# Kernel optimization log

Measured on AMD Instinct MI355X. Metric: run time of the kernel, lower is better.

## Reference

```python
import jax, jax.numpy as jnp
import numpy as np

N_HEADS = 16

def _rope_tables(L, head_dim, dtype):
    inv_freq = 1.0 / (10000.0 ** (jnp.arange(0, head_dim, 2, dtype=jnp.float32) / head_dim))
    t = jnp.arange(L, dtype=jnp.float32)
    freqs = jnp.outer(t, inv_freq)            # [L, head_dim/2]
    emb = jnp.concatenate([freqs, freqs], -1)  # [L, head_dim]
    return jnp.cos(emb).astype(dtype), jnp.sin(emb).astype(dtype)

def _apply_rope(x, cos, sin):
    # x: [B, L, H, hd]; cos/sin: [1, L, 1, hd]
    half = x.shape[-1] // 2
    x1, x2 = x[..., :half], x[..., half:]
    x_rot = jnp.concatenate([-x2, x1], -1)
    return x * cos + x_rot * sin

def setup_inputs() -> dict:
    key = jax.random.key(0)
    ks = jax.random.split(key, 5)
    D = 1024
    s = 0.02
    return {
        "x": jax.random.normal(ks[0], (4, 2048, D), jnp.float32),
        "w_qkv": jax.random.normal(ks[1], (3 * D, D), jnp.float32) * s,
        "b_qkv": jax.random.normal(ks[2], (3 * D,), jnp.float32) * s,
        "w_out": jax.random.normal(ks[3], (D, D), jnp.float32) * s,
        "b_out": jax.random.normal(ks[4], (D,), jnp.float32) * s,
    }

def reference(x, w_qkv, b_qkv, w_out, b_out):
    B, L, D = x.shape
    H = N_HEADS
    hd = D // H
    scale = hd ** -0.5
    qkv = (x @ w_qkv.T + b_qkv).reshape(B, L, 3, H, hd)
    q, k, v = qkv[:, :, 0], qkv[:, :, 1], qkv[:, :, 2]  # [B,L,H,hd]
    cos, sin = _rope_tables(L, hd, x.dtype)
    cos = cos[None, :, None, :]
    sin = sin[None, :, None, :]
    q = _apply_rope(q, cos, sin)
    k = _apply_rope(k, cos, sin)
    # [B,H,L,L] scores, non-causal softmax
    attn = jnp.einsum('blhd,bmhd->bhlm', q, k) * scale
    attn = jax.nn.softmax(attn, axis=-1)
    out = jnp.einsum('bhlm,bmhd->blhd', attn, v).reshape(B, L, D)
    return out @ w_out.T + b_out
```

## Files before the change

kernel.cpp:

```cpp
#include <hip/hip_runtime.h>
#include <stdint.h>

typedef __attribute__((ext_vector_type(4))) float f32x4;
typedef __attribute__((ext_vector_type(8))) short bf16x8;
typedef __attribute__((ext_vector_type(4))) short s16x4;
typedef __attribute__((ext_vector_type(4))) float fp32x4;

#define QSCALE 0.18033688f

__device__ __forceinline__ short f2bf(float f) {
    union { float f; unsigned u; } v; v.f = f;
    unsigned u = v.u;
    unsigned r = u + 0x7fffu + ((u >> 16) & 1u);
    return (short)(r >> 16);
}
__device__ __forceinline__ unsigned cvtpk(float a, float b) {
    unsigned r;
    asm("v_cvt_pk_bf16_f32 %0, %1, %2" : "=v"(r) : "v"(a), "v"(b));
    return r;
}

__device__ __forceinline__ void gld_lds16(const void* g, void* l) {
    __builtin_amdgcn_global_load_lds(
        (const __attribute__((address_space(1))) unsigned int*)(uintptr_t)g,
        (__attribute__((address_space(3))) unsigned int*)(uintptr_t)l,
        16, 0, 0);
}

__global__ __launch_bounds__(256) void prep_kernel(const float* __restrict__ x,
                                                   const float* __restrict__ wq,
                                                   const float* __restrict__ wo,
                                                   short* __restrict__ xb,
                                                   short* __restrict__ wqb,
                                                   short* __restrict__ wob,
                                                   float* __restrict__ tab) {
    int bid = blockIdx.x, tid = threadIdx.x;
    if (bid < 6144) {
        const float* in; short* out; int base;
        if (bid < 4096)      { in = x;  out = xb;  base = bid; }
        else if (bid < 5632) { in = wq; out = wqb; base = bid - 4096; }
        else                 { in = wo; out = wob; base = bid - 5632; }
        int idx = (base * 256 + tid) * 8;
        fp32x4 a = *(const fp32x4*)&in[idx];
        fp32x4 b = *(const fp32x4*)&in[idx + 4];
        union { unsigned w[4]; bf16x8 v; } u;
        u.w[0] = cvtpk(a[0], a[1]); u.w[1] = cvtpk(a[2], a[3]);
        u.w[2] = cvtpk(b[0], b[1]); u.w[3] = cvtpk(b[2], b[3]);
        *(bf16x8*)&out[idx] = u.v;
    } else {
        int idx = (bid - 6144) * 256 + tid;
        int l = idx >> 5, d = idx & 31;
        float inv = expf(-(float)d / 32.f * logf(10000.f));
        float ang = (float)l * inv;
        tab[idx * 2 + 0] = cosf(ang);
        tab[idx * 2 + 1] = sinf(ang);
    }
}

template<int MODE>
__global__ __launch_bounds__(512, 2)
void gemm_bt(const short* __restrict__ A,
             const short* __restrict__ B,
             const float* __restrict__ bias,
             void* __restrict__ Cout,
             short* __restrict__ VTout,
             const float* __restrict__ tab,
             int M, int N, int K) {
    __shared__ short lds[3 * 24576];
    const int tid = threadIdx.x;
    const int lane = tid & 63, wave = tid >> 6;
    const int i15 = lane & 15, g = lane >> 4;
    const int wr = wave >> 1, wc = wave & 1;

    const int nbx = gridDim.x;
    const int nwg = nbx * gridDim.y;
    int bid = blockIdx.y * nbx + blockIdx.x;
    int sw = (bid & 7) * (nwg >> 3) + (bid >> 3);
    const int m0 = (sw / nbx) * 256;
    const int n0 = (sw % nbx) * 128;

    const int xr3 = i15 & 3, xb2 = (i15 >> 2) & 1;
    const int cLo = g ^ xr3;
    const int aoff0 = (wr * 64 + i15) * 64 + (xb2 * 4 + cLo) * 8;
    const int aoff1 = (wr * 64 + i15) * 64 + ((1 ^ xb2) * 4 + cLo) * 8;
    const int boff0 = (wc * 64 + i15) * 64 + (xb2 * 4 + cLo) * 8;
    const int boff1 = (wc * 64 + i15) * 64 + ((1 ^ xb2) * 4 + cLo) * 8;

    const int srow = tid >> 3;
    const int ss = (tid & 7) ^ (srow & 7);
    const short* a0 = A + (size_t)(m0 + srow) * K + ss * 8;
    const short* a1 = a0 + (size_t)64 * K;
    const short* a2 = a0 + (size_t)128 * K;
    const short* a3 = a0 + (size_t)192 * K;
    const short* b0 = B + (size_t)(n0 + srow) * K + ss * 8;
    const short* b1 = b0 + (size_t)64 * K;

#define ST_A(slot, r, p) do { gld_lds16(p, lds + (slot) * 24576 + ((r) * 512 + wave * 64) * 8); p += 64; } while (0)
#define ST_B(slot, r, p) do { gld_lds16(p, lds + (slot) * 24576 + 16384 + ((r) * 512 + wave * 64) * 8); p += 64; } while (0)

    ST_A(0, 0, a0); ST_A(0, 1, a1); ST_B(0, 0, b0);
    ST_A(0, 2, a2); ST_A(0, 3, a3); ST_B(0, 1, b1);
    ST_A(1, 0, a0); ST_A(1, 1, a1); ST_B(1, 0, b0);
    ST_A(1, 2, a2); ST_A(1, 3, a3); ST_B(1, 1, b1);

    f32x4 acc[4][4] = {};
    const int NT = K >> 6;
    int slc = 0;

    for (int T = 0; T < NT; ++T) {
        int stslot = slc + 2; if (stslot >= 3) stslot -= 3;
        if (T == NT - 1) asm volatile("s_waitcnt vmcnt(0)" ::: "memory");
        else             asm volatile("s_waitcnt vmcnt(6)" ::: "memory");
        __builtin_amdgcn_s_barrier();
        __builtin_amdgcn_sched_barrier(0);

        if (T + 2 < NT) {
            ST_A(stslot, 0, a0); ST_A(stslot, 1, a1);
            ST_A(stslot, 2, a2); ST_A(stslot, 3, a3);
            ST_B(stslot, 0, b0); ST_B(stslot, 1, b1);
        }

        const short* As_ = lds + slc * 24576;
        const short* Bs_ = As_ + 16384;
        bf16x8 af[4][2], bfr[4][2];
#pragma unroll
        for (int m = 0; m < 4; ++m) {
            af[m][0] = *(const bf16x8*)&As_[aoff0 + m * 1024];
            af[m][1] = *(const bf16x8*)&As_[aoff1 + m * 1024];
        }
#pragma unroll
        for (int n = 0; n < 4; ++n) {
            bfr[n][0] = *(const bf16x8*)&Bs_[boff0 + n * 1024];
            bfr[n][1] = *(const bf16x8*)&Bs_[boff1 + n * 1024];
        }
        __builtin_amdgcn_s_setprio(1);
#pragma unroll
        for (int m = 0; m < 4; ++m)
#pragma unroll
            for (int n = 0; n < 4; ++n)
#pragma unroll
                for (int ks = 0; ks < 2; ++ks)
                    acc[m][n] = __builtin_amdgcn_mfma_f32_16x16x32_bf16(af[m][ks], bfr[n][ks], acc[m][n], 0, 0, 0);
        __builtin_amdgcn_s_setprio(0);

        slc = (slc == 2) ? 0 : slc + 1;
    }
#undef ST_A
#undef ST_B

    if (MODE == 0) {
#pragma unroll
        for (int m = 0; m < 4; ++m)
#pragma unroll
            for (int n = 0; n < 4; ++n) {
                int col = n0 + wc * 64 + n * 16 + i15;
                float bcol = bias[col];
#pragma unroll
                for (int j = 0; j < 4; ++j) {
                    int row = m0 + wr * 64 + m * 16 + g * 4 + j;
                    ((float*)Cout)[(size_t)row * N + col] = acc[m][n][j] + bcol;
                }
            }
    } else {
        const int sec = n0 >> 10;
        if (sec < 2) {
            const float qs = (sec == 0) ? QSCALE : 1.0f;
            short* out = (short*)Cout;
#pragma unroll
            for (int m = 0; m < 4; ++m) {
#pragma unroll
                for (int pp = 0; pp < 2; ++pp) {
                    int d = pp * 16 + i15;
                    int collo = n0 + wc * 64 + pp * 16 + i15;
                    float blo = bias[collo], bhi = bias[collo + 32];
#pragma unroll
                    for (int j = 0; j < 4; ++j) {
                        int row = m0 + wr * 64 + m * 16 + g * 4 + j;
                        int l = row & 2047;
                        float2 cs = *(const float2*)&tab[(l * 32 + d) * 2];
                        float x1 = acc[m][pp][j] + blo;
                        float x2 = acc[m][pp + 2][j] + bhi;
                        out[(size_t)row * 3072 + collo]      = f2bf((x1 * cs.x - x2 * cs.y) * qs);
                        out[(size_t)row * 3072 + collo + 32] = f2bf((x2 * cs.x + x1 * cs.y) * qs);
                    }
                }
            }
        } else {
#pragma unroll
            for (int m = 0; m < 4; ++m) {
                int rbase = m0 + wr * 64 + m * 16 + g * 4;
                int lbase = rbase & 2047, bidx = rbase >> 11;
#pragma unroll
                for (int n = 0; n < 4; ++n) {
                    int vcol = (n0 - 2048) + wc * 64 + n * 16 + i15;
                    int h = vcol >> 6, d = vcol & 63;
                    float bb = bias[n0 + wc * 64 + n * 16 + i15];
                    union { unsigned w[2]; s16x4 v; } u;
                    u.w[0] = cvtpk(acc[m][n][0] + bb, acc[m][n][1] + bb);
                    u.w[1] = cvtpk(acc[m][n][2] + bb, acc[m][n][3] + bb);
                    *(s16x4*)&VTout[((size_t)(bidx * 16 + h) * 64 + d) * 2048 + lbase] = u.v;
                }
            }
        }
    }
}

__global__ __launch_bounds__(512, 8) void attn_kernel(const short* __restrict__ qkv,
                                                      const short* __restrict__ VT,
                                                      short* __restrict__ O) {
    __shared__ short Ks[2][64 * 64];
    __shared__ short Vs[2][64 * 64];
    int orig = blockIdx.x;
    int xcd = orig & 7, idx = orig >> 3;
    int bh = xcd * 8 + (idx >> 4), qt = idx & 15;
    int b = bh >> 4, h = bh & 15;
    int tid = threadIdx.x, lane = tid & 63, wave = tid >> 6;
    int i15 = lane & 15, g = lane >> 4;
    int q0 = qt * 128;

    size_t qrow = (size_t)(b * 2048 + q0 + wave * 16 + i15);
    bf16x8 qf[2];
    qf[0] = *(const bf16x8*)&qkv[qrow * 3072 + h * 64 + 0  + g * 8];
    qf[1] = *(const bf16x8*)&qkv[qrow * 3072 + h * 64 + 32 + g * 8];

    bf16x8 onesf;
#pragma unroll
    for (int e = 0; e < 8; ++e) onesf[e] = (short)0x3F80;

    const int srow = tid >> 3, ss8 = (tid & 7) ^ (srow & 7);
    const int sprow = (srow & 0x23) | ((srow & 0x10) >> 2) | ((srow & 0x0C) << 1);
    const short* kp = qkv + (size_t)(b * 2048) * 3072 + 1024 + h * 64
                      + (size_t)sprow * 3072 + ss8 * 8;
    const short* vp = VT + (size_t)bh * 64 * 2048 + (size_t)srow * 2048 + ss8 * 8;

    const int xr3 = i15 & 3, xb2 = (i15 >> 2) & 1;
    const int cLo = g ^ xr3;
    const int o0 = i15 * 64 + (xb2 * 4 + cLo) * 8;
    const int o1 = i15 * 64 + ((1 ^ xb2) * 4 + cLo) * 8;

    f32x4 acc_o[4] = {};
    f32x4 acc_l = {0.f, 0.f, 0.f, 0.f};

#define STAGE(bk, bv)                                        \
    do {                                                     \
        gld_lds16(kp, (bk) + wave * 512);                    \
        gld_lds16(vp, (bv) + wave * 512);                    \
        kp += 64 * 3072;                                     \
        vp += 64;                                            \
    } while (0)

    STAGE(Ks[0], Vs[0]);

    for (int t = 0; t < 32; ++t) {
        const int cur = t & 1;
        if (t > 0) {
            __builtin_amdgcn_s_barrier();
            __builtin_amdgcn_sched_barrier(0);
        }
        if (t + 1 < 32) {
            STAGE(Ks[cur ^ 1], Vs[cur ^ 1]);
            asm volatile("s_waitcnt vmcnt(2)" ::: "memory");
        } else {
            asm volatile("s_waitcnt vmcnt(0)" ::: "memory");
        }
        __builtin_amdgcn_s_barrier();
        __builtin_amdgcn_sched_barrier(0);

        const short* ks = Ks[cur];
        const short* vs = Vs[cur];

        f32x4 sa[4] = {};
        __builtin_amdgcn_s_setprio(1);
#pragma unroll
        for (int kb = 0; kb < 2; ++kb) {
            const int ko = kb ? o1 : o0;
#pragma unroll
            for (int jb = 0; jb < 4; ++jb) {
                bf16x8 kf = *(const bf16x8*)&ks[ko + jb * 1024];
                sa[jb] = __builtin_amdgcn_mfma_f32_16x16x32_bf16(kf, qf[kb], sa[jb], 0, 0, 0);
            }
        }
        __builtin_amdgcn_s_setprio(0);

        float p[4][4];
#pragma unroll
        for (int jb = 0; jb < 4; ++jb)
#pragma unroll
            for (int r = 0; r < 4; ++r)
                p[jb][r] = __builtin_amdgcn_exp2f(sa[jb][r]);

        bf16x8 pf[2];
#pragma unroll
        for (int kb = 0; kb < 2; ++kb) {
            union { unsigned w[4]; bf16x8 v; } u;
            u.w[0] = cvtpk(p[2 * kb][0],     p[2 * kb][1]);
            u.w[1] = cvtpk(p[2 * kb][2],     p[2 * kb][3]);
            u.w[2] = cvtpk(p[2 * kb + 1][0], p[2 * kb + 1][1]);
            u.w[3] = cvtpk(p[2 * kb + 1][2], p[2 * kb + 1][3]);
            pf[kb] = u.v;
        }

        __builtin_amdgcn_s_setprio(1);
#pragma unroll
        for (int db = 0; db < 4; ++db) {
#pragma unroll
            for (int kb = 0; kb < 2; ++kb) {
                bf16x8 vf = *(const bf16x8*)&vs[(kb ? o1 : o0) + db * 1024];
                acc_o[db] = __builtin_amdgcn_mfma_f32_16x16x32_bf16(pf[kb], vf, acc_o[db], 0, 0, 0);
            }
        }
        acc_l = __builtin_amdgcn_mfma_f32_16x16x32_bf16(pf[0], onesf, acc_l, 0, 0, 0);
        acc_l = __builtin_amdgcn_mfma_f32_16x16x32_bf16(pf[1], onesf, acc_l, 0, 0, 0);
        __builtin_amdgcn_s_setprio(0);
    }
#undef STAGE

    float linv4[4];
#pragma unroll
    for (int r = 0; r < 4; ++r) linv4[r] = 1.f / acc_l[r];
#pragma unroll
    for (int db = 0; db < 4; ++db) {
        int ocol = h * 64 + db * 16 + i15;
#pragma unroll
        for (int r = 0; r < 4; ++r) {
            int orow = b * 2048 + q0 + wave * 16 + g * 4 + r;
            O[(size_t)orow * 1024 + ocol] = f2bf(acc_o[db][r] * linv4[r]);
        }
    }
}

extern "C" void kernel_launch(void* const* d_in, const int* in_sizes, int n_in,
                              void* d_out, int out_size, void* d_ws, size_t ws_size,
                              hipStream_t stream) {
    const float* x     = (const float*)d_in[0];
    const float* w_qkv = (const float*)d_in[1];
    const float* b_qkv = (const float*)d_in[2];
    const float* w_out = (const float*)d_in[3];
    const float* b_out = (const float*)d_in[4];

    char* ws = (char*)d_ws;
    short* qkvb = (short*)(ws);
    short* xb   = (short*)(ws + 50331648);
    short* wqb  = (short*)(ws + 67108864);
    short* wob  = (short*)(ws + 73400320);
    short* VT   = (short*)(ws + 75497472);
    float* rt   = (float*)(ws + 92274688);
    short* Ob   = xb;

    prep_kernel<<<6400, 256, 0, stream>>>(x, w_qkv, w_out, xb, wqb, wob, rt);

    gemm_bt<1><<<dim3(24, 32), 512, 0, stream>>>(xb, wqb, b_qkv, qkvb, VT, rt, 8192, 3072, 1024);
    attn_kernel<<<1024, 512, 0, stream>>>(qkvb, VT, Ob);
    gemm_bt<0><<<dim3(8, 32), 512, 0, stream>>>(Ob, wob, b_out, d_out, nullptr, nullptr, 8192, 1024, 1024);
}
```

Baseline: 171.1 us.

## Shrink GEMM tiles to 128x128 with 4 waves and give attention waves 32 query rows

The GEMM moves from 512-thread 256x128 tiles with a 3-slot LDS ring to 256-thread 128x128 tiles with double buffering, and the grid doubles in M. The attention kernel now runs 4 waves per block, each handling two 16-row query groups, so every K/V fragment read from LDS is reused twice. Each thread stages twice as many K/V rows per tile. The aim is better reuse and a better occupancy/latency balance, at the cost of more registers per wave and shallower prefetch in the GEMM.

```diff
diff --git a/kernel.cpp b/kernel.cpp
--- a/kernel.cpp
+++ b/kernel.cpp
@@ -58,7 +58,7 @@
 }
 
 template<int MODE>
-__global__ __launch_bounds__(512, 2)
+__global__ __launch_bounds__(256, 2)
 void gemm_bt(const short* __restrict__ A,
              const short* __restrict__ B,
              const float* __restrict__ bias,
@@ -66,7 +66,7 @@
              short* __restrict__ VTout,
              const float* __restrict__ tab,
              int M, int N, int K) {
-    __shared__ short lds[3 * 24576];
+    __shared__ short lds[2 * 16384];
     const int tid = threadIdx.x;
     const int lane = tid & 63, wave = tid >> 6;
     const int i15 = lane & 15, g = lane >> 4;
@@ -76,7 +76,7 @@
     const int nwg = nbx * gridDim.y;
     int bid = blockIdx.y * nbx + blockIdx.x;
     int sw = (bid & 7) * (nwg >> 3) + (bid >> 3);
-    const int m0 = (sw / nbx) * 256;
+    const int m0 = (sw / nbx) * 128;
     const int n0 = (sw % nbx) * 128;
 
     const int xr3 = i15 & 3, xb2 = (i15 >> 2) & 1;
@@ -89,39 +89,50 @@
     const int srow = tid >> 3;
     const int ss = (tid & 7) ^ (srow & 7);
     const short* a0 = A + (size_t)(m0 + srow) * K + ss * 8;
-    const short* a1 = a0 + (size_t)64 * K;
-    const short* a2 = a0 + (size_t)128 * K;
-    const short* a3 = a0 + (size_t)192 * K;
+    const short* a1 = a0 + (size_t)32 * K;
+    const short* a2 = a0 + (size_t)64 * K;
+    const short* a3 = a0 + (size_t)96 * K;
     const short* b0 = B + (size_t)(n0 + srow) * K + ss * 8;
-    const short* b1 = b0 + (size_t)64 * K;
-
-#define ST_A(slot, r, p) do { gld_lds16(p, lds + (slot) * 24576 + ((r) * 512 + wave * 64) * 8); p += 64; } while (0)
-#define ST_B(slot, r, p) do { gld_lds16(p, lds + (slot) * 24576 + 16384 + ((r) * 512 + wave * 64) * 8); p += 64; } while (0)
-
-    ST_A(0, 0, a0); ST_A(0, 1, a1); ST_B(0, 0, b0);
-    ST_A(0, 2, a2); ST_A(0, 3, a3); ST_B(0, 1, b1);
-    ST_A(1, 0, a0); ST_A(1, 1, a1); ST_B(1, 0, b0);
-    ST_A(1, 2, a2); ST_A(1, 3, a3); ST_B(1, 1, b1);
+    const short* b1 = b0 + (size_t)32 * K;
+    const short* b2 = b0 + (size_t)64 * K;
+    const short* b3 = b0 + (size_t)96 * K;
+
+#define STAGE(slot)                                                       \
+    do {                                                                  \
+        gld_lds16(a0, lds + (slot) * 16384 + 0 * 2048 + wave * 512);      \
+        gld_lds16(a1, lds + (slot) * 16384 + 1 * 2048 + wave * 512);      \
+        gld_lds16(a2, lds + (slot) * 16384 + 2 * 2048 + wave * 512);      \
+        gld_lds16(a3, lds + (slot) * 16384 + 3 * 2048 + wave * 512);      \
+        gld_lds16(b0, lds + (slot) * 16384 + 8192 + 0 * 2048 + wave * 512); \
+        gld_lds16(b1, lds + (slot) * 16384 + 8192 + 1 * 2048 + wave * 512); \
+        gld_lds16(b2, lds + (slot) * 16384 + 8192 + 2 * 2048 + wave * 512); \
+        gld_lds16(b3, lds + (slot) * 16384 + 8192 + 3 * 2048 + wave * 512); \
+        a0 += 64; a1 += 64; a2 += 64; a3 += 64;                           \
+        b0 += 64; b1 += 64; b2 += 64; b3 += 64;                           \
+    } while (0)
+
+    STAGE(0);
 
     f32x4 acc[4][4] = {};
     const int NT = K >> 6;
-    int slc = 0;
 
     for (int T = 0; T < NT; ++T) {
-        int stslot = slc + 2; if (stslot >= 3) stslot -= 3;
-        if (T == NT - 1) asm volatile("s_waitcnt vmcnt(0)" ::: "memory");
-        else             asm volatile("s_waitcnt vmcnt(6)" ::: "memory");
+        const int cur = T & 1;
+        if (T > 0) {
+            __builtin_amdgcn_s_barrier();
+            __builtin_amdgcn_sched_barrier(0);
+        }
+        if (T + 1 < NT) {
+            STAGE(cur ^ 1);
+            asm volatile("s_waitcnt vmcnt(8)" ::: "memory");
+        } else {
+            asm volatile("s_waitcnt vmcnt(0)" ::: "memory");
+        }
         __builtin_amdgcn_s_barrier();
         __builtin_amdgcn_sched_barrier(0);
 
-        if (T + 2 < NT) {
-            ST_A(stslot, 0, a0); ST_A(stslot, 1, a1);
-            ST_A(stslot, 2, a2); ST_A(stslot, 3, a3);
-            ST_B(stslot, 0, b0); ST_B(stslot, 1, b1);
-        }
-
-        const short* As_ = lds + slc * 24576;
-        const short* Bs_ = As_ + 16384;
+        const short* As_ = lds + cur * 16384;
+        const short* Bs_ = As_ + 8192;
         bf16x8 af[4][2], bfr[4][2];
 #pragma unroll
         for (int m = 0; m < 4; ++m) {
@@ -142,11 +153,8 @@
                 for (int ks = 0; ks < 2; ++ks)
                     acc[m][n] = __builtin_amdgcn_mfma_f32_16x16x32_bf16(af[m][ks], bfr[n][ks], acc[m][n], 0, 0, 0);
         __builtin_amdgcn_s_setprio(0);
-
-        slc = (slc == 2) ? 0 : slc + 1;
-    }
-#undef ST_A
-#undef ST_B
+    }
+#undef STAGE
 
     if (MODE == 0) {
 #pragma unroll
@@ -205,7 +213,7 @@
     }
 }
 
-__global__ __launch_bounds__(512, 8) void attn_kernel(const short* __restrict__ qkv,
+__global__ __launch_bounds__(256, 4) void attn_kernel(const short* __restrict__ qkv,
                                                       const short* __restrict__ VT,
                                                       short* __restrict__ O) {
     __shared__ short Ks[2][64 * 64];
@@ -218,35 +226,46 @@
     int i15 = lane & 15, g = lane >> 4;
     int q0 = qt * 128;
 
-    size_t qrow = (size_t)(b * 2048 + q0 + wave * 16 + i15);
-    bf16x8 qf[2];
-    qf[0] = *(const bf16x8*)&qkv[qrow * 3072 + h * 64 + 0  + g * 8];
-    qf[1] = *(const bf16x8*)&qkv[qrow * 3072 + h * 64 + 32 + g * 8];
+    size_t qbase = (size_t)(b * 2048 + q0 + wave * 32);
+    bf16x8 qf[2][2];
+#pragma unroll
+    for (int qg = 0; qg < 2; ++qg) {
+        qf[qg][0] = *(const bf16x8*)&qkv[(qbase + qg * 16 + i15) * 3072 + h * 64 + 0  + g * 8];
+        qf[qg][1] = *(const bf16x8*)&qkv[(qbase + qg * 16 + i15) * 3072 + h * 64 + 32 + g * 8];
+    }
 
     bf16x8 onesf;
 #pragma unroll
     for (int e = 0; e < 8; ++e) onesf[e] = (short)0x3F80;
 
-    const int srow = tid >> 3, ss8 = (tid & 7) ^ (srow & 7);
-    const int sprow = (srow & 0x23) | ((srow & 0x10) >> 2) | ((srow & 0x0C) << 1);
-    const short* kp = qkv + (size_t)(b * 2048) * 3072 + 1024 + h * 64
-                      + (size_t)sprow * 3072 + ss8 * 8;
-    const short* vp = VT + (size_t)bh * 64 * 2048 + (size_t)srow * 2048 + ss8 * 8;
+    const int srow = tid >> 3;
+    const int ss8 = (tid & 7) ^ (srow & 7);
+    const int pr0 = (srow & 0x23) | ((srow & 0x10) >> 2) | ((srow & 0x0C) << 1);
+    const int sr1 = srow + 32;
+    const int pr1 = (sr1 & 0x23) | ((sr1 & 0x10) >> 2) | ((sr1 & 0x0C) << 1);
+    const short* kb_ = qkv + (size_t)(b * 2048) * 3072 + 1024 + h * 64 + ss8 * 8;
+    const short* kp0 = kb_ + (size_t)pr0 * 3072;
+    const short* kp1 = kb_ + (size_t)pr1 * 3072;
+    const short* vb_ = VT + (size_t)bh * 64 * 2048 + ss8 * 8;
+    const short* vp0 = vb_ + (size_t)srow * 2048;
+    const short* vp1 = vb_ + (size_t)sr1 * 2048;
 
     const int xr3 = i15 & 3, xb2 = (i15 >> 2) & 1;
     const int cLo = g ^ xr3;
     const int o0 = i15 * 64 + (xb2 * 4 + cLo) * 8;
     const int o1 = i15 * 64 + ((1 ^ xb2) * 4 + cLo) * 8;
 
-    f32x4 acc_o[4] = {};
-    f32x4 acc_l = {0.f, 0.f, 0.f, 0.f};
+    f32x4 acc_o[2][4] = {};
+    f32x4 acc_l[2] = {};
 
 #define STAGE(bk, bv)                                        \
     do {                                                     \
-        gld_lds16(kp, (bk) + wave * 512);                    \
-        gld_lds16(vp, (bv) + wave * 512);                    \
-        kp += 64 * 3072;                                     \
-        vp += 64;                                            \
+        gld_lds16(kp0, (bk) + wave * 512);                   \
+        gld_lds16(kp1, (bk) + 2048 + wave * 512);            \
+        gld_lds16(vp0, (bv) + wave * 512);                   \
+        gld_lds16(vp1, (bv) + 2048 + wave * 512);            \
+        kp0 += (size_t)64 * 3072; kp1 += (size_t)64 * 3072;  \
+        vp0 += 64; vp1 += 64;                                \
     } while (0)
 
     STAGE(Ks[0], Vs[0]);
@@ -259,7 +278,7 @@
         }
         if (t + 1 < 32) {
             STAGE(Ks[cur ^ 1], Vs[cur ^ 1]);
-            asm volatile("s_waitcnt vmcnt(2)" ::: "memory");
+            asm volatile("s_waitcnt vmcnt(4)" ::: "memory");
         } else {
             asm volatile("s_waitcnt vmcnt(0)" ::: "memory");
         }
@@ -269,35 +288,40 @@
         const short* ks = Ks[cur];
         const short* vs = Vs[cur];
 
-        f32x4 sa[4] = {};
+        f32x4 sa[2][4] = {};
         __builtin_amdgcn_s_setprio(1);
 #pragma unroll
         for (int kb = 0; kb < 2; ++kb) {
             const int ko = kb ? o1 : o0;
-#pragma unroll
-            for (int jb = 0; jb < 4; ++jb) {
-                bf16x8 kf = *(const bf16x8*)&ks[ko + jb * 1024];
-                sa[jb] = __builtin_amdgcn_mfma_f32_16x16x32_bf16(kf, qf[kb], sa[jb], 0, 0, 0);
-            }
+            bf16x8 kf[4];
+#pragma unroll
+            for (int jb = 0; jb < 4; ++jb) kf[jb] = *(const bf16x8*)&ks[ko + jb * 1024];
+#pragma unroll
+            for (int qg = 0; qg < 2; ++qg)
+#pragma unroll
+                for (int jb = 0; jb < 4; ++jb)
+                    sa[qg][jb] = __builtin_amdgcn_mfma_f32_16x16x32_bf16(kf[jb], qf[qg][kb], sa[qg][jb], 0, 0, 0);
         }
         __builtin_amdgcn_s_setprio(0);
 
-        float p[4][4];
-#pragma unroll
-        for (int jb = 0; jb < 4; ++jb)
-#pragma unroll
-            for (int r = 0; r < 4; ++r)
-                p[jb][r] = __builtin_amdgcn_exp2f(sa[jb][r]);
-
-        bf16x8 pf[2];
-#pragma unroll
-        for (int kb = 0; kb < 2; ++kb) {
-            union { unsigned w[4]; bf16x8 v; } u;
-            u.w[0] = cvtpk(p[2 * kb][0],     p[2 * kb][1]);
-            u.w[1] = cvtpk(p[2 * kb][2],     p[2 * kb][3]);
-            u.w[2] = cvtpk(p[2 * kb + 1][0], p[2 * kb + 1][1]);
-            u.w[3] = cvtpk(p[2 * kb + 1][2], p[2 * kb + 1][3]);
-            pf[kb] = u.v;
+        bf16x8 pf[2][2];
+#pragma unroll
+        for (int qg = 0; qg < 2; ++qg) {
+            float p[4][4];
+#pragma unroll
+            for (int jb = 0; jb < 4; ++jb)
+#pragma unroll
+                for (int r = 0; r < 4; ++r)
+                    p[jb][r] = __builtin_amdgcn_exp2f(sa[qg][jb][r]);
+#pragma unroll
+            for (int kb = 0; kb < 2; ++kb) {
+                union { unsigned w[4]; bf16x8 v; } u;
+                u.w[0] = cvtpk(p[2 * kb][0],     p[2 * kb][1]);
+                u.w[1] = cvtpk(p[2 * kb][2],     p[2 * kb][3]);
+                u.w[2] = cvtpk(p[2 * kb + 1][0], p[2 * kb + 1][1]);
+                u.w[3] = cvtpk(p[2 * kb + 1][2], p[2 * kb + 1][3]);
+                pf[qg][kb] = u.v;
+            }
         }
 
         __builtin_amdgcn_s_setprio(1);
@@ -306,25 +330,33 @@
 #pragma unroll
             for (int kb = 0; kb < 2; ++kb) {
                 bf16x8 vf = *(const bf16x8*)&vs[(kb ? o1 : o0) + db * 1024];
-                acc_o[db] = __builtin_amdgcn_mfma_f32_16x16x32_bf16(pf[kb], vf, acc_o[db], 0, 0, 0);
-            }
-        }
-        acc_l = __builtin_amdgcn_mfma_f32_16x16x32_bf16(pf[0], onesf, acc_l, 0, 0, 0);
-        acc_l = __builtin_amdgcn_mfma_f32_16x16x32_bf16(pf[1], onesf, acc_l, 0, 0, 0);
+#pragma unroll
+                for (int qg = 0; qg < 2; ++qg)
+                    acc_o[qg][db] = __builtin_amdgcn_mfma_f32_16x16x32_bf16(pf[qg][kb], vf, acc_o[qg][db], 0, 0, 0);
+            }
+        }
+#pragma unroll
+        for (int qg = 0; qg < 2; ++qg) {
+            acc_l[qg] = __builtin_amdgcn_mfma_f32_16x16x32_bf16(pf[qg][0], onesf, acc_l[qg], 0, 0, 0);
+            acc_l[qg] = __builtin_amdgcn_mfma_f32_16x16x32_bf16(pf[qg][1], onesf, acc_l[qg], 0, 0, 0);
+        }
         __builtin_amdgcn_s_setprio(0);
     }
 #undef STAGE
 
-    float linv4[4];
-#pragma unroll
-    for (int r = 0; r < 4; ++r) linv4[r] = 1.f / acc_l[r];
-#pragma unroll
-    for (int db = 0; db < 4; ++db) {
-        int ocol = h * 64 + db * 16 + i15;
-#pragma unroll
-        for (int r = 0; r < 4; ++r) {
-            int orow = b * 2048 + q0 + wave * 16 + g * 4 + r;
-            O[(size_t)orow * 1024 + ocol] = f2bf(acc_o[db][r] * linv4[r]);
+#pragma unroll
+    for (int qg = 0; qg < 2; ++qg) {
+        float linv4[4];
+#pragma unroll
+        for (int r = 0; r < 4; ++r) linv4[r] = 1.f / acc_l[qg][r];
+#pragma unroll
+        for (int db = 0; db < 4; ++db) {
+            int ocol = h * 64 + db * 16 + i15;
+#pragma unroll
+            for (int r = 0; r < 4; ++r) {
+                size_t orow = qbase + qg * 16 + g * 4 + r;
+                O[orow * 1024 + ocol] = f2bf(acc_o[qg][db][r] * linv4[r]);
+            }
         }
     }
 }
@@ -349,7 +381,7 @@
 
     prep_kernel<<<6400, 256, 0, stream>>>(x, w_qkv, w_out, xb, wqb, wob, rt);
 
-    gemm_bt<1><<<dim3(24, 32), 512, 0, stream>>>(xb, wqb, b_qkv, qkvb, VT, rt, 8192, 3072, 1024);
-    attn_kernel<<<1024, 512, 0, stream>>>(qkvb, VT, Ob);
-    gemm_bt<0><<<dim3(8, 32), 512, 0, stream>>>(Ob, wob, b_out, d_out, nullptr, nullptr, 8192, 1024, 1024);
-}
+    gemm_bt<1><<<dim3(24, 64), 256, 0, stream>>>(xb, wqb, b_qkv, qkvb, VT, rt, 8192, 3072, 1024);
+    attn_kernel<<<1024, 256, 0, stream>>>(qkvb, VT, Ob);
+    gemm_bt<0><<<dim3(8, 64), 256, 0, stream>>>(Ob, wob, b_out, d_out, nullptr, nullptr, 8192, 1024, 1024);
+}
```

After: 162.4 us, median of 2. 5.1% less time.
